# Kernel tuning notes

Hardware: AMD Instinct MI355X
Metric: run time of the kernel (lower is better)

The kernel has to match this reference:

```python
import jax, jax.numpy as jnp
import numpy as np

B = 32; SEQ = 900; GRID = 30; PFX = 16; D = 512
H = 8; HD = 64; WS = 3; SS = 1
NW = (GRID // WS) ** 2; N = WS * WS
INTER = 1536  # find_multiple(round(4.0*512*2/3), 256)
EPS = 1e-5
SCALE = HD ** -0.5


def _rel_pos_index():
    coords = np.stack(np.meshgrid(np.arange(WS), np.arange(WS), indexing='ij')).reshape(2, -1)
    rel = (coords[:, :, None] - coords[:, None, :]).transpose(1, 2, 0).copy()
    rel[:, :, 0] += WS - 1
    rel[:, :, 1] += WS - 1
    rel[:, :, 0] *= 2 * WS - 1
    return rel.sum(-1)  # [N, N]


def _attn_mask():
    img = np.zeros((GRID, GRID))
    cnt = 0
    sl = (slice(0, -WS), slice(-WS, -SS), slice(-SS, None))
    for h in sl:
        for w in sl:
            img[h, w] = cnt
            cnt += 1
    mw = img.reshape(GRID // WS, WS, GRID // WS, WS).transpose(0, 2, 1, 3).reshape(-1, N)
    diff = mw[:, None, :] - mw[:, :, None]
    return np.where(diff != 0, -100.0, 0.0).astype(np.float32)  # [nW, N, N]


REL_IDX = _rel_pos_index()
MASK = _attn_mask()


def rms_norm(x):
    xf = x.astype(jnp.float32)
    v = jnp.mean(xf * xf, -1, keepdims=True)
    return (xf * jax.lax.rsqrt(v + EPS)).astype(x.dtype)


def swiglu(x, gu_w, down_w):
    gu = x @ gu_w.T
    gate, up = gu[..., :INTER], gu[..., INTER:]
    return (jax.nn.silu(gate) * up) @ down_w.T


def setup_inputs() -> dict:
    key = jax.random.key(0)
    ks = jax.random.split(key, 8)
    s = 0.02
    return {
        'hidden_states': jax.random.normal(ks[0], (B, PFX + SEQ, D), jnp.float32),
        'qkv_w': jax.random.normal(ks[1], (3 * D, D), jnp.float32) * s,
        'qkv_b': jnp.zeros((3 * D,), jnp.float32),
        'proj_w': jax.random.normal(ks[2], (D, D), jnp.float32) * s,
        'proj_b': jnp.zeros((D,), jnp.float32),
        'rel_bias': jax.random.normal(ks[3], ((2 * WS - 1) ** 2, H), jnp.float32) * s,
        'gu_w': jax.random.normal(ks[4], (2 * INTER, D), jnp.float32) * s,
        'down_w': jax.random.normal(ks[5], (D, INTER), jnp.float32) * s,
        'pgu_w': jax.random.normal(ks[6], (2 * INTER, D), jnp.float32) * s,
        'pdown_w': jax.random.normal(ks[7], (D, INTER), jnp.float32) * s,
    }


def reference(hidden_states, qkv_w, qkv_b, proj_w, proj_b, rel_bias, gu_w, down_w, pgu_w, pdown_w):
    hs = hidden_states
    prefix = hs[:, :PFX]                                     # [B, 16, D]
    grid = hs[:, PFX:] + jnp.mean(prefix, 1, keepdims=True)  # broadcast prefix mean
    x = grid.reshape(B, GRID, GRID, D)
    residual = x
    # cyclic shift
    x = jnp.roll(x, (-SS, -SS), (1, 2))
    # window partition -> [B*nW, N, D]
    xw = x.reshape(B, GRID // WS, WS, GRID // WS, WS, D).transpose(0, 1, 3, 2, 4, 5).reshape(B * NW, N, D)
    qkv = (xw @ qkv_w.T + qkv_b).reshape(B * NW, N, 3, H, HD).transpose(2, 0, 3, 1, 4)
    q, k, v = qkv[0] * SCALE, qkv[1], qkv[2]                 # [B*nW, H, N, HD]
    attn = jnp.einsum('whid,whjd->whij', q, k)
    bias = rel_bias[jnp.asarray(REL_IDX).reshape(-1)].reshape(N, N, H).transpose(2, 0, 1)
    attn = attn + bias[None]
    attn = attn.reshape(B, NW, H, N, N) + jnp.asarray(MASK)[None, :, None]
    attn = jax.nn.softmax(attn.reshape(B * NW, H, N, N), -1)
    out = jnp.einsum('whij,whjd->whid', attn, v).transpose(0, 2, 1, 3).reshape(B * NW, N, D)
    out = out @ proj_w.T + proj_b
    # window reverse + reverse shift
    x = out.reshape(B, GRID // WS, GRID // WS, WS, WS, D).transpose(0, 1, 3, 2, 4, 5).reshape(B, GRID, GRID, D)
    x = jnp.roll(x, (SS, SS), (1, 2))
    x = rms_norm(residual.reshape(B, SEQ, D) + x.reshape(B, SEQ, D))
    prefix = rms_norm(prefix + swiglu(prefix, pgu_w, pdown_w))
    hs = jnp.concatenate([prefix, x], 1)
    return rms_norm(hs + swiglu(hs, gu_w, down_w))
```

## Files before the change

### kernel.cpp

```cpp
#include <hip/hip_runtime.h>
#include <cstdint>
#include <cstddef>

typedef float f32x4 __attribute__((ext_vector_type(4)));
typedef short s16x8 __attribute__((ext_vector_type(8)));
typedef short s16x4 __attribute__((ext_vector_type(4)));

#define DEV static __device__ __forceinline__

DEV float bf2f(short s) {
  union { unsigned u; float f; } c;
  c.u = ((unsigned)(unsigned short)s) << 16;
  return c.f;
}
DEV short f2bf(float f) {
  union { float f; unsigned u; } c;
  c.f = f;
  unsigned r = c.u + 0x7fffu + ((c.u >> 16) & 1u);
  return (short)(r >> 16);
}
DEV float wave_allsum(float v) {
#pragma unroll
  for (int off = 32; off > 0; off >>= 1) v += __shfl_xor(v, off, 64);
  return v;
}
DEV void gload_lds16(const void* g, void* l) {
  __builtin_amdgcn_global_load_lds(
      (const __attribute__((address_space(1))) void*)g,
      (__attribute__((address_space(3))) void*)l, 16, 0, 0);
}
DEV float silu_f(float g) { return g / (1.f + __expf(-g)); }

DEV int xcd_swizzle(int orig, int nwg) {
  int q = nwg >> 3, r = nwg & 7;
  int xcd = orig & 7, pos = orig >> 3;
  return (xcd < r ? xcd * (q + 1) : r * (q + 1) + (xcd - r) * q) + pos;
}

DEV void sync_phase() {
  asm volatile("s_waitcnt vmcnt(0)" ::: "memory");
  __builtin_amdgcn_s_barrier();
  __builtin_amdgcn_sched_barrier(0);
}

enum { EPI_BF16 = 0, EPI_BIAS_BF16 = 1, EPI_SCATTER = 4, EPI_GU = 6 };

template <int EPI>
__global__ __launch_bounds__(512, 2) void gemm8(
    const short* __restrict__ A, const short* __restrict__ W,
    const float* __restrict__ bias, void* __restrict__ outp,
    int M, int N, int K)
{
  __shared__ short lds[65536];
  const int tid = threadIdx.x;
  const int wid = tid >> 6, lane = tid & 63;
  const int wr = wid >> 2, wc = wid & 3;
  const int nwg = gridDim.x * gridDim.y;
  const int orig = blockIdx.y * gridDim.x + blockIdx.x;
  const int wg = xcd_swizzle(orig, nwg);
  const int bx = wg % gridDim.x, by = wg / gridDim.x;
  const int row0 = by * 256;
  const int c0 = bx * 256;

  f32x4 acc[8][4];
#pragma unroll
  for (int m = 0; m < 8; ++m)
#pragma unroll
    for (int n = 0; n < 4; ++n) acc[m][n] = f32x4{0.f, 0.f, 0.f, 0.f};

  const int srow = tid >> 3;
  const int k8s = (tid & 7) ^ (srow & 7);
  const short* aub[4];
  const short* bub[4];
#pragma unroll
  for (int u = 0; u < 4; ++u) {
    aub[u] = A + (size_t)(row0 + u * 64 + srow) * K + k8s * 8;
    bub[u] = W + (size_t)(c0 + u * 64 + srow) * K + k8s * 8;
  }
  const int ldw = wid * 512;

#define SA(d, u, kt) gload_lds16(aub[u] + (kt), &lds[(d)*16384 + (u)*4096 + ldw])
#define SB(d, u, kt) gload_lds16(bub[u] + (kt), &lds[32768 + (d)*16384 + (u)*4096 + ldw])
#define GATE(VN)                                              \
  asm volatile("s_waitcnt vmcnt(" #VN ")" ::: "memory");      \
  __builtin_amdgcn_s_barrier();                               \
  __builtin_amdgcn_sched_barrier(0);

  const int kg0 = (lane >> 4) ^ (lane & 7);
  const int kg1 = (4 + (lane >> 4)) ^ (lane & 7);
  const int aoff = (wr * 128 + (lane & 15)) * 64;
  const int boff = 32768 + (wc * 64 + (lane & 15)) * 64;

#define READ_B(d)                                                              \
  _Pragma("unroll") for (int n = 0; n < 4; ++n) {                              \
    bfr[0][n] = *(const s16x8*)&lds[(d)*16384 + boff + n * 1024 + kg0 * 8];    \
    bfr[1][n] = *(const s16x8*)&lds[(d)*16384 + boff + n * 1024 + kg1 * 8];    \
  }
#define DO_PHASE(d, p)                                                         \
  do {                                                                         \
    s16x8 a00 = *(const s16x8*)&lds[(d)*16384 + aoff + (2*(p))*1024 + kg0*8];  \
    s16x8 a01 = *(const s16x8*)&lds[(d)*16384 + aoff + (2*(p))*1024 + kg1*8];  \
    s16x8 a10 = *(const s16x8*)&lds[(d)*16384 + aoff + (2*(p)+1)*1024 + kg0*8];\
    s16x8 a11 = *(const s16x8*)&lds[(d)*16384 + aoff + (2*(p)+1)*1024 + kg1*8];\
    __builtin_amdgcn_s_setprio(1);                                             \
    _Pragma("unroll") for (int n = 0; n < 4; ++n)                              \
      acc[2*(p)][n] = __builtin_amdgcn_mfma_f32_16x16x32_bf16(a00, bfr[0][n], acc[2*(p)][n], 0, 0, 0); \
    _Pragma("unroll") for (int n = 0; n < 4; ++n)                              \
      acc[2*(p)+1][n] = __builtin_amdgcn_mfma_f32_16x16x32_bf16(a10, bfr[0][n], acc[2*(p)+1][n], 0, 0, 0); \
    _Pragma("unroll") for (int n = 0; n < 4; ++n)                              \
      acc[2*(p)][n] = __builtin_amdgcn_mfma_f32_16x16x32_bf16(a01, bfr[1][n], acc[2*(p)][n], 0, 0, 0); \
    _Pragma("unroll") for (int n = 0; n < 4; ++n)                              \
      acc[2*(p)+1][n] = __builtin_amdgcn_mfma_f32_16x16x32_bf16(a11, bfr[1][n], acc[2*(p)+1][n], 0, 0, 0); \
    __builtin_amdgcn_s_setprio(0);                                             \
  } while (0)

  SB(0, 0, 0); SB(0, 1, 0); SB(0, 2, 0); SB(0, 3, 0);
  SA(0, 0, 0); SA(0, 2, 0); SA(0, 1, 0); SA(0, 3, 0);

  const int NT = K >> 6;
  for (int t = 0; t < NT - 1; ++t) {
    const int d = t & 1, d1 = d ^ 1;
    const int kn = (t + 1) * 64;
    s16x8 bfr[2][4];
    SB(d1, 0, kn); SB(d1, 1, kn);
    GATE(4);
    READ_B(d);
    DO_PHASE(d, 0);
    SB(d1, 2, kn); SB(d1, 3, kn);
    DO_PHASE(d, 1);
    SA(d1, 0, kn); SA(d1, 2, kn);
    GATE(6);
    DO_PHASE(d, 2);
    SA(d1, 1, kn); SA(d1, 3, kn);
    DO_PHASE(d, 3);
  }
  {
    const int d = (NT - 1) & 1;
    s16x8 bfr[2][4];
    GATE(2);
    READ_B(d);
    DO_PHASE(d, 0);
    DO_PHASE(d, 1);
    GATE(0);
    DO_PHASE(d, 2);
    DO_PHASE(d, 3);
  }
#undef SA
#undef SB
#undef READ_B
#undef DO_PHASE
#undef GATE

  const int li = lane >> 4, lc = lane & 15;
#pragma unroll
  for (int m = 0; m < 8; ++m) {
#pragma unroll
    for (int i = 0; i < 4; ++i) {
      int gr = row0 + wr * 128 + m * 16 + li * 4 + i;
      if (gr >= M) continue;
      size_t orow;
      if (EPI == EPI_SCATTER) {
        int b = gr / 900, rem = gr % 900;
        int w = rem / 9, n_ = rem % 9;
        int wi = w / 10, wj = w % 10;
        int ii = n_ / 3, jj = n_ % 3;
        int gy = wi * 3 + ii + 1; if (gy >= 30) gy -= 30;
        int gx = wj * 3 + jj + 1; if (gx >= 30) gx -= 30;
        orow = (size_t)b * 900 + gy * 30 + gx;
      } else {
        orow = (size_t)gr;
      }
#pragma unroll
      for (int n = 0; n < 4; ++n) {
        int gc = c0 + wc * 64 + n * 16 + lc;
        float v = acc[m][n][i];
        if (EPI == EPI_BIAS_BF16 || EPI == EPI_SCATTER) v += bias[gc];
        ((short*)outp)[orow * (size_t)N + gc] = f2bf(v);
      }
    }
  }
}

__global__ __launch_bounds__(256, 2) void gemm8gu(
    const short* __restrict__ A, const short* __restrict__ Wg,
    const short* __restrict__ Wu, short* __restrict__ outp, int M, int K)
{
  __shared__ short lds[40960];
  const int tid = threadIdx.x;
  const int w = tid >> 6, lane = tid & 63;
  const int wr = w >> 1, wc = w & 1;
  const int nwg = gridDim.x * gridDim.y;
  const int orig = blockIdx.y * gridDim.x + blockIdx.x;
  const int wg = xcd_swizzle(orig, nwg);
  const int bx = wg % gridDim.x, by = wg / gridDim.x;
  const int row0 = by * 64;
  const int colg = bx * 128;

  f32x4 accg[2][4], accu[2][4];
#pragma unroll
  for (int m = 0; m < 2; ++m)
#pragma unroll
    for (int n = 0; n < 4; ++n) {
      accg[m][n] = f32x4{0.f, 0.f, 0.f, 0.f};
      accu[m][n] = f32x4{0.f, 0.f, 0.f, 0.f};
    }

  const short* aptr[2];
#pragma unroll
  for (int i = 0; i < 2; ++i) {
    int r = (i * 4 + w) * 8 + (lane >> 3);
    int k8 = (lane & 7) ^ (r & 7);
    aptr[i] = A + (size_t)(row0 + r) * K + k8 * 8;
  }
  const short* bptr[8];
#pragma unroll
  for (int j = 0; j < 8; ++j) {
    int br = (j * 4 + w) * 8 + (lane >> 3);
    int k8 = (lane & 7) ^ (br & 7);
    bptr[j] = (br < 128 ? Wg + (size_t)(colg + br) * K
                        : Wu + (size_t)(colg + br - 128) * K) + k8 * 8;
  }

#define SAV(d, kt)                                                         \
  do {                                                                     \
    gload_lds16(aptr[0] + (kt), &lds[(d)*4096 + w * 512]);                 \
    gload_lds16(aptr[1] + (kt), &lds[(d)*4096 + 2048 + w * 512]);          \
  } while (0)
#define SBG(d, kt)                                                         \
  do {                                                                     \
    _Pragma("unroll") for (int j = 0; j < 4; ++j)                          \
        gload_lds16(bptr[j] + (kt), &lds[8192 + (d)*16384 + (j*4 + w)*512]);\
  } while (0)
#define SBU(d, kt)                                                         \
  do {                                                                     \
    _Pragma("unroll") for (int j = 4; j < 8; ++j)                          \
        gload_lds16(bptr[j] + (kt), &lds[8192 + (d)*16384 + (j*4 + w)*512]);\
  } while (0)
#define GATE(VN)                                              \
  asm volatile("s_waitcnt vmcnt(" #VN ")" ::: "memory");      \
  __builtin_amdgcn_s_barrier();                               \
  __builtin_amdgcn_sched_barrier(0);

  const int kg0 = (lane >> 4) ^ (lane & 7);
  const int kg1 = (4 + (lane >> 4)) ^ (lane & 7);
  const int aoff = (wr * 32 + (lane & 15)) * 64;
  const int bgoff = 8192 + (wc * 64 + (lane & 15)) * 64;
  const int buoff = bgoff + 8192;

#define READ_A(d)                                                              \
  _Pragma("unroll") for (int m = 0; m < 2; ++m) {                              \
    af[0][m] = *(const s16x8*)&lds[(d)*4096 + aoff + m * 1024 + kg0 * 8];      \
    af[1][m] = *(const s16x8*)&lds[(d)*4096 + aoff + m * 1024 + kg1 * 8];      \
  }
#define READ_BF(d, BOFF, BF)                                                   \
  _Pragma("unroll") for (int n = 0; n < 4; ++n) {                              \
    BF[0][n] = *(const s16x8*)&lds[(d)*16384 + (BOFF) + n * 1024 + kg0 * 8];   \
    BF[1][n] = *(const s16x8*)&lds[(d)*16384 + (BOFF) + n * 1024 + kg1 * 8];   \
  }
#define MMH(BF, g, ACC)                                                        \
  do {                                                                         \
    __builtin_amdgcn_s_setprio(1);                                             \
    _Pragma("unroll") for (int m = 0; m < 2; ++m)                              \
        _Pragma("unroll") for (int n = 0; n < 4; ++n)                          \
            ACC[m][n] = __builtin_amdgcn_mfma_f32_16x16x32_bf16(               \
                af[g][m], BF[g][n], ACC[m][n], 0, 0, 0);                       \
    __builtin_amdgcn_s_setprio(0);                                             \
  } while (0)

  SAV(0, 0); SBG(0, 0); SBU(0, 0);

  const int NT = K >> 6;
  for (int t = 0; t < NT - 1; ++t) {
    const int d = t & 1, d1 = d ^ 1;
    const int kn = (t + 1) * 64;
    s16x8 af[2][2], bg[2][4], bu[2][4];
    GATE(4);
    READ_A(d);
    READ_BF(d, bgoff, bg);
    MMH(bg, 0, accg);
    SAV(d1, kn);
    MMH(bg, 1, accg);
    SBG(d1, kn);
    GATE(6);
    READ_BF(d, buoff, bu);
    MMH(bu, 0, accu);
    SBU(d1, kn);
    MMH(bu, 1, accu);
  }
  {
    const int d = (NT - 1) & 1;
    s16x8 af[2][2], bg[2][4], bu[2][4];
    GATE(4);
    READ_A(d);
    READ_BF(d, bgoff, bg);
    MMH(bg, 0, accg);
    MMH(bg, 1, accg);
    GATE(0);
    READ_BF(d, buoff, bu);
    MMH(bu, 0, accu);
    MMH(bu, 1, accu);
  }
#undef SAV
#undef SBG
#undef SBU
#undef READ_A
#undef READ_BF
#undef MMH
#undef GATE

  const int li = lane >> 4, lc = lane & 15;
#pragma unroll
  for (int m = 0; m < 2; ++m) {
#pragma unroll
    for (int i = 0; i < 4; ++i) {
      int gr = row0 + wr * 32 + m * 16 + li * 4 + i;
      if (gr >= M) continue;
#pragma unroll
      for (int n = 0; n < 4; ++n) {
        int gc = colg + wc * 64 + n * 16 + lc;
        outp[(size_t)gr * 1536 + gc] = f2bf(silu_f(accg[m][n][i]) * accu[m][n][i]);
      }
    }
  }
}

template <int EPI>
__global__ __launch_bounds__(256) void gemm2(
    const short* __restrict__ A, const short* __restrict__ W,
    const short* __restrict__ Wu, const float* __restrict__ bias,
    void* __restrict__ outp, int M, int N, int K)
{
  __shared__ short As0[8192], Bs0[8192];
  __shared__ short As1[8192], Bs1[8192];
  const int tid = threadIdx.x;
  const int wave = tid >> 6, lane = tid & 63;
  const int nwg = gridDim.x * gridDim.y;
  const int orig = blockIdx.y * gridDim.x + blockIdx.x;
  const int wg = xcd_swizzle(orig, nwg);
  const int bx = wg % gridDim.x, by = wg / gridDim.x;
  const int row0 = by * 128;
  const int col0 = (EPI == EPI_GU) ? bx * 64 : bx * 128;
  const int wr = wave >> 1, wc = wave & 1;

  f32x4 acc[4][4];
#pragma unroll
  for (int m = 0; m < 4; ++m)
#pragma unroll
    for (int n = 0; n < 4; ++n) acc[m][n] = f32x4{0.f, 0.f, 0.f, 0.f};

  const short* aptr[4];
  const short* bptr[4];
  int ldst[4];
#pragma unroll
  for (int i = 0; i < 4; ++i) {
    int e = i * 2048 + tid * 8;
    int srow = e >> 6;
    int skg = ((e >> 3) & 7) ^ (srow & 7);
    aptr[i] = A + (size_t)(row0 + srow) * K + skg * 8;
    if (EPI == EPI_GU)
      bptr[i] = (srow < 64 ? W + (size_t)(col0 + srow) * K
                           : Wu + (size_t)(col0 + srow - 64) * K) + skg * 8;
    else
      bptr[i] = W + (size_t)(col0 + srow) * K + skg * 8;
    ldst[i] = i * 2048 + wave * 512;
  }

#define STAGE(AS, BS, KT)                                   \
  do {                                                      \
    _Pragma("unroll") for (int i = 0; i < 4; ++i)           \
        gload_lds16(aptr[i] + (KT), &AS[ldst[i]]);          \
    _Pragma("unroll") for (int i = 0; i < 4; ++i)           \
        gload_lds16(bptr[i] + (KT), &BS[ldst[i]]);          \
  } while (0)

#define COMPUTE(AS, BS)                                                        \
  do {                                                                         \
    _Pragma("unroll") for (int ks = 0; ks < 2; ++ks) {                         \
      s16x8 af[4], bfr[4];                                                     \
      _Pragma("unroll") for (int m = 0; m < 4; ++m) {                          \
        int row = wr * 64 + m * 16 + (lane & 15);                              \
        int kg = (ks * 4 + (lane >> 4)) ^ (row & 7);                           \
        af[m] = *(const s16x8*)&AS[row * 64 + kg * 8];                         \
      }                                                                        \
      _Pragma("unroll") for (int n = 0; n < 4; ++n) {                          \
        int brow = (EPI == EPI_GU)                                             \
                       ? ((n < 2 ? wc * 32 + n * 16                            \
                                 : 64 + wc * 32 + (n - 2) * 16) + (lane & 15)) \
                       : (wc * 64 + n * 16 + (lane & 15));                     \
        int kg = (ks * 4 + (lane >> 4)) ^ (brow & 7);                          \
        bfr[n] = *(const s16x8*)&BS[brow * 64 + kg * 8];                       \
      }                                                                        \
      _Pragma("unroll") for (int m = 0; m < 4; ++m)                            \
          _Pragma("unroll") for (int n = 0; n < 4; ++n)                        \
              acc[m][n] = __builtin_amdgcn_mfma_f32_16x16x32_bf16(             \
                  af[m], bfr[n], acc[m][n], 0, 0, 0);                          \
    }                                                                          \
  } while (0)

  STAGE(As0, Bs0, 0);
  sync_phase();
  for (int kt = 0; kt < K; kt += 128) {
    STAGE(As1, Bs1, kt + 64);
    COMPUTE(As0, Bs0);
    sync_phase();
    if (kt + 128 < K) STAGE(As0, Bs0, kt + 128);
    COMPUTE(As1, Bs1);
    if (kt + 128 < K) sync_phase();
  }
#undef STAGE
#undef COMPUTE

  const int lr = (lane >> 4) * 4, lc = lane & 15;
#pragma unroll
  for (int m = 0; m < 4; ++m) {
#pragma unroll
    for (int i = 0; i < 4; ++i) {
      int gr = row0 + wr * 64 + m * 16 + lr + i;
      if (EPI == EPI_GU) {
#pragma unroll
        for (int n = 0; n < 2; ++n) {
          int gc = col0 + wc * 32 + n * 16 + lc;
          float v = silu_f(acc[m][n][i]) * acc[m][n + 2][i];
          ((short*)outp)[(size_t)gr * N + gc] = f2bf(v);
        }
      } else {
#pragma unroll
        for (int n = 0; n < 4; ++n) {
          int gc = col0 + wc * 64 + n * 16 + lc;
          ((short*)outp)[(size_t)gr * N + gc] = f2bf(acc[m][n][i]);
        }
      }
    }
  }
}

__global__ __launch_bounds__(256) void cvt_all_kernel(
    const float* __restrict__ s_qkv, const float* __restrict__ s_proj,
    const float* __restrict__ s_gu, const float* __restrict__ s_down,
    const float* __restrict__ s_pgu, const float* __restrict__ s_pdown,
    short* __restrict__ dst) {
  int i = blockIdx.x * 256 + threadIdx.x;
  if (i >= 1441792) return;
  const float* src;
  int base;
  if (i < 262144) {
    if (i < 196608) { src = s_qkv; base = 0; }
    else            { src = s_proj; base = 196608; }
  } else if (i < 851968) {
    if (i < 655360) { src = s_gu; base = 262144; }
    else            { src = s_down; base = 655360; }
  } else {
    if (i < 1245184) { src = s_pgu; base = 851968; }
    else             { src = s_pdown; base = 1245184; }
  }
  f32x4 v = *(const f32x4*)(src + (size_t)(i - base) * 4);
  s16x4 o;
#pragma unroll
  for (int e = 0; e < 4; ++e) o[e] = f2bf(v[e]);
  *(s16x4*)(dst + (size_t)i * 4) = o;
}

__global__ __launch_bounds__(256) void prefix_cvt_kernel(const float* __restrict__ hs,
                                                         short* __restrict__ dst) {
  int i = blockIdx.x * 256 + threadIdx.x;
  if (i >= 512 * 128) return;
  int r = i >> 7, c4 = i & 127;
  int b = r >> 4, t = r & 15;
  f32x4 v = *(const f32x4*)(hs + ((size_t)b * 916 + t) * 512 + c4 * 4);
  s16x4 o;
#pragma unroll
  for (int e = 0; e < 4; ++e) o[e] = f2bf(v[e]);
  *(s16x4*)(dst + (size_t)r * 512 + c4 * 4) = o;
}

__global__ __launch_bounds__(512) void mean_kernel(const float* __restrict__ hs,
                                                   float* __restrict__ m) {
  int b = blockIdx.x, d = threadIdx.x;
  float s = 0.f;
#pragma unroll
  for (int t = 0; t < 16; ++t) s += hs[((size_t)b * 916 + t) * 512 + d];
  m[b * 512 + d] = s * (1.f / 16.f);
}

__global__ __launch_bounds__(256) void prep_kernel(const float* __restrict__ hs,
                                                   const float* __restrict__ m,
                                                   short* __restrict__ xw) {
  int idx = blockIdx.x * 256 + threadIdx.x;
  if (idx >= 32 * 900 * 128) return;
  int c4 = idx & 127;
  int row = idx >> 7;
  int b = row / 900, rem = row % 900;
  int gy = rem / 30, gx = rem % 30;
  f32x4 v = *(const f32x4*)(hs + ((size_t)b * 916 + 16 + rem) * 512 + c4 * 4);
  f32x4 mm = *(const f32x4*)(m + b * 512 + c4 * 4);
  v += mm;
  int ry = gy + 29; if (ry >= 30) ry -= 30;
  int rx = gx + 29; if (rx >= 30) rx -= 30;
  int wi = ry / 3, ii = ry % 3, wj = rx / 3, jj = rx % 3;
  size_t xrow = (size_t)((b * 100 + wi * 10 + wj) * 9 + ii * 3 + jj);
  s16x4 o;
#pragma unroll
  for (int e = 0; e < 4; ++e) o[e] = f2bf(v[e]);
  *(s16x4*)(xw + xrow * 512 + c4 * 4) = o;
}

__global__ __launch_bounds__(256) void attn_kernel(const short* __restrict__ qkv,
                                                   const float* __restrict__ rel_bias,
                                                   short* __restrict__ outp) {
  __shared__ short sq[9 * 512];
  __shared__ short sk[9 * 512];
  __shared__ short sv[9 * 512];
  __shared__ float sS[648];
  const int wlin = blockIdx.x;
  const int w = wlin % 100;
  const int wi = w / 10, wj = w % 10;
  const int tid = threadIdx.x;
  const short* base = qkv + (size_t)wlin * 9 * 1536;
  for (int idx = tid; idx < 1728; idx += 256) {
    int n = idx / 192, c8 = idx % 192;
    s16x8 v = *(const s16x8*)(base + (size_t)n * 1536 + c8 * 8);
    int which = c8 >> 6;
    short* dst = (which == 0) ? sq : (which == 1) ? sk : sv;
    *(s16x8*)(dst + n * 512 + (c8 & 63) * 8) = v;
  }
  __syncthreads();
  for (int idx = tid; idx < 648; idx += 256) {
    int h = idx / 81, r = idx % 81, i = r / 9, j = r % 9;
    const short* qp = sq + i * 512 + h * 64;
    const short* kp = sk + j * 512 + h * 64;
    float dot = 0.f;
#pragma unroll
    for (int c = 0; c < 8; ++c) {
      s16x8 qv = *(const s16x8*)(qp + c * 8);
      s16x8 kv = *(const s16x8*)(kp + c * 8);
#pragma unroll
      for (int e = 0; e < 8; ++e) dot += bf2f(qv[e]) * bf2f(kv[e]);
    }
    float s = dot * 0.125f;
    int ia = i / 3, ja = i % 3, ib = j / 3, jb = j % 3;
    s += rel_bias[(5 * (ia - ib + 2) + (ja - jb + 2)) * 8 + h];
    int ra = wi * 3 + ia, ca = wj * 3 + ja, rb = wi * 3 + ib, cb = wj * 3 + jb;
    int rga = (ra < 27) ? 0 : (ra < 29) ? 1 : 2;
    int cga = (ca < 27) ? 0 : (ca < 29) ? 1 : 2;
    int rgb = (rb < 27) ? 0 : (rb < 29) ? 1 : 2;
    int cgb = (cb < 27) ? 0 : (cb < 29) ? 1 : 2;
    if (rga * 3 + cga != rgb * 3 + cgb) s -= 100.f;
    sS[idx] = s;
  }
  __syncthreads();
  if (tid < 72) {
    float* row = sS + tid * 9;
    float mx = row[0];
#pragma unroll
    for (int j = 1; j < 9; ++j) mx = fmaxf(mx, row[j]);
    float e[9], sum = 0.f;
#pragma unroll
    for (int j = 0; j < 9; ++j) { e[j] = __expf(row[j] - mx); sum += e[j]; }
    float inv = 1.f / sum;
#pragma unroll
    for (int j = 0; j < 9; ++j) row[j] = e[j] * inv;
  }
  __syncthreads();
  for (int idx = tid; idx < 576; idx += 256) {
    int h = idx / 72, r = idx % 72, i = r / 8, d8 = r % 8;
    const float* p = sS + (h * 9 + i) * 9;
    float a[8] = {0, 0, 0, 0, 0, 0, 0, 0};
#pragma unroll
    for (int j = 0; j < 9; ++j) {
      float pj = p[j];
      s16x8 vv = *(const s16x8*)(sv + j * 512 + h * 64 + d8 * 8);
#pragma unroll
      for (int e = 0; e < 8; ++e) a[e] += pj * bf2f(vv[e]);
    }
    s16x8 o;
#pragma unroll
    for (int e = 0; e < 8; ++e) o[e] = f2bf(a[e]);
    *(s16x8*)(outp + ((size_t)wlin * 9 + i) * 512 + h * 64 + d8 * 8) = o;
  }
}

__global__ __launch_bounds__(256) void addnorm1_kernel(const short* __restrict__ xw,
                                                       const short* __restrict__ p,
                                                       float* __restrict__ out,
                                                       short* __restrict__ hsb) {
  int row = blockIdx.x * 4 + (threadIdx.x >> 6);
  int lane = threadIdx.x & 63;
  int b_ = row / 900, rem = row % 900;
  int gy = rem / 30, gx = rem % 30;
  int ry = gy + 29; if (ry >= 30) ry -= 30;
  int rx = gx + 29; if (rx >= 30) rx -= 30;
  size_t xrow = (size_t)((b_ * 100 + (ry / 3) * 10 + rx / 3) * 9 + (ry % 3) * 3 + rx % 3);
  s16x8 a8 = *(const s16x8*)(xw + xrow * 512 + lane * 8);
  s16x8 b8 = *(const s16x8*)(p + (size_t)row * 512 + lane * 8);
  float x[8];
  float ss = 0.f;
#pragma unroll
  for (int e = 0; e < 8; ++e) {
    x[e] = bf2f(a8[e]) + bf2f(b8[e]);
    ss += x[e] * x[e];
  }
  ss = wave_allsum(ss);
  float sc = rsqrtf(ss * (1.f / 512.f) + 1e-5f);
  size_t orow = ((size_t)b_ * 916 + 16 + rem) * 512 + lane * 8;
  s16x8 o;
#pragma unroll
  for (int e = 0; e < 8; ++e) {
    x[e] *= sc;
    o[e] = f2bf(x[e]);
  }
  *(f32x4*)(out + orow) = f32x4{x[0], x[1], x[2], x[3]};
  *(f32x4*)(out + orow + 4) = f32x4{x[4], x[5], x[6], x[7]};
  *(s16x8*)(hsb + orow) = o;
}

__global__ __launch_bounds__(256) void prefix_addnorm_kernel(const float* __restrict__ hs,
                                                             const short* __restrict__ pd,
                                                             float* __restrict__ out,
                                                             short* __restrict__ hsb) {
  int r = blockIdx.x * 4 + (threadIdx.x >> 6);
  int lane = threadIdx.x & 63;
  int b = r >> 4, t = r & 15;
  size_t orow = ((size_t)b * 916 + t) * 512 + lane * 8;
  f32x4 a0 = *(const f32x4*)(hs + orow);
  f32x4 a1 = *(const f32x4*)(hs + orow + 4);
  s16x8 d8 = *(const s16x8*)(pd + (size_t)r * 512 + lane * 8);
  float x[8];
  float ss = 0.f;
#pragma unroll
  for (int e = 0; e < 8; ++e) {
    x[e] = (e < 4 ? a0[e] : a1[e - 4]) + bf2f(d8[e]);
    ss += x[e] * x[e];
  }
  ss = wave_allsum(ss);
  float sc = rsqrtf(ss * (1.f / 512.f) + 1e-5f);
  s16x8 o;
#pragma unroll
  for (int e = 0; e < 8; ++e) {
    x[e] *= sc;
    o[e] = f2bf(x[e]);
  }
  *(f32x4*)(out + orow) = f32x4{x[0], x[1], x[2], x[3]};
  *(f32x4*)(out + orow + 4) = f32x4{x[4], x[5], x[6], x[7]};
  *(s16x8*)(hsb + orow) = o;
}

__global__ __launch_bounds__(256) void final_addnorm_kernel(const short* __restrict__ dn,
                                                            float* __restrict__ io) {
  int row = blockIdx.x * 4 + (threadIdx.x >> 6);
  int lane = threadIdx.x & 63;
  size_t off = (size_t)row * 512 + lane * 8;
  f32x4 a0 = *(const f32x4*)(io + off);
  f32x4 a1 = *(const f32x4*)(io + off + 4);
  s16x8 d8 = *(const s16x8*)(dn + off);
  float x[8];
  float ss = 0.f;
#pragma unroll
  for (int e = 0; e < 8; ++e) {
    x[e] = (e < 4 ? a0[e] : a1[e - 4]) + bf2f(d8[e]);
    ss += x[e] * x[e];
  }
  ss = wave_allsum(ss);
  float sc = rsqrtf(ss * (1.f / 512.f) + 1e-5f);
#pragma unroll
  for (int e = 0; e < 8; ++e) x[e] *= sc;
  *(f32x4*)(io + off) = f32x4{x[0], x[1], x[2], x[3]};
  *(f32x4*)(io + off + 4) = f32x4{x[4], x[5], x[6], x[7]};
}

static constexpr size_t OFF_WQKV   = 0;
static constexpr size_t OFF_WPROJ  = 1572864;
static constexpr size_t OFF_WGU    = 2097152;
static constexpr size_t OFF_WDOWN  = 5242880;
static constexpr size_t OFF_WPGU   = 6815744;
static constexpr size_t OFF_WPDOWN = 9961472;
static constexpr size_t OFF_MEAN   = 11534336;
static constexpr size_t OFF_PREFB  = 11599872;
static constexpr size_t OFF_PINTER = 13697024;
static constexpr size_t OFF_PDOUT  = 15269888;
static constexpr size_t OFF_XW     = 16777216;
static constexpr size_t OFF_QKV    = 46399488;
static constexpr size_t OFF_ATTNO  = 134873088;
static constexpr size_t OFF_PROJS  = OFF_QKV;
static constexpr size_t OFF_INTER  = OFF_XW;
static constexpr size_t OFF_HSB    = 164364288;
static constexpr size_t OFF_DNOUT  = OFF_ATTNO;

extern "C" void kernel_launch(void* const* d_in, const int* in_sizes, int n_in,
                              void* d_out, int out_size, void* d_ws, size_t ws_size,
                              hipStream_t stream) {
  const float* hs      = (const float*)d_in[0];
  const float* qkv_w   = (const float*)d_in[1];
  const float* qkv_b   = (const float*)d_in[2];
  const float* proj_w  = (const float*)d_in[3];
  const float* proj_b  = (const float*)d_in[4];
  const float* rel_b   = (const float*)d_in[5];
  const float* gu_w    = (const float*)d_in[6];
  const float* down_w  = (const float*)d_in[7];
  const float* pgu_w   = (const float*)d_in[8];
  const float* pdown_w = (const float*)d_in[9];

  char* ws = (char*)d_ws;
  short* Wqkv   = (short*)(ws + OFF_WQKV);
  short* Wproj  = (short*)(ws + OFF_WPROJ);
  short* Wgu    = (short*)(ws + OFF_WGU);
  short* Wdown  = (short*)(ws + OFF_WDOWN);
  short* Wpgu   = (short*)(ws + OFF_WPGU);
  short* Wpdown = (short*)(ws + OFF_WPDOWN);
  float* meanb  = (float*)(ws + OFF_MEAN);
  short* prefb  = (short*)(ws + OFF_PREFB);
  short* pinter = (short*)(ws + OFF_PINTER);
  short* pdout  = (short*)(ws + OFF_PDOUT);
  short* xw     = (short*)(ws + OFF_XW);
  short* qkvb   = (short*)(ws + OFF_QKV);
  short* attno  = (short*)(ws + OFF_ATTNO);
  short* projs  = (short*)(ws + OFF_PROJS);
  short* interb = (short*)(ws + OFF_INTER);
  short* hsb    = (short*)(ws + OFF_HSB);
  short* dnout  = (short*)(ws + OFF_DNOUT);
  float* outf   = (float*)d_out;

  cvt_all_kernel<<<5632, 256, 0, stream>>>(qkv_w, proj_w, gu_w, down_w,
                                           pgu_w, pdown_w, (short*)ws);
  prefix_cvt_kernel<<<256, 256, 0, stream>>>(hs, prefb);

  mean_kernel<<<32, 512, 0, stream>>>(hs, meanb);
  prep_kernel<<<14400, 256, 0, stream>>>(hs, meanb, xw);

  gemm8<EPI_BIAS_BF16><<<dim3(6, 113), 512, 0, stream>>>(
      xw, Wqkv, qkv_b, qkvb, 28800, 1536, 512);
  attn_kernel<<<3200, 256, 0, stream>>>(qkvb, rel_b, attno);

  gemm8<EPI_SCATTER><<<dim3(2, 113), 512, 0, stream>>>(
      attno, Wproj, proj_b, projs, 28800, 512, 512);
  addnorm1_kernel<<<7200, 256, 0, stream>>>(xw, projs, outf, hsb);

  gemm2<EPI_GU><<<dim3(24, 4), 256, 0, stream>>>(
      prefb, Wpgu, Wpgu + 1536 * 512, nullptr, pinter, 512, 1536, 512);
  gemm2<EPI_BF16><<<dim3(4, 4), 256, 0, stream>>>(
      pinter, Wpdown, nullptr, nullptr, pdout, 512, 512, 1536);
  prefix_addnorm_kernel<<<128, 256, 0, stream>>>(hs, pdout, outf, hsb);

  gemm8gu<<<dim3(12, 458), 256, 0, stream>>>(
      hsb, Wgu, Wgu + 1536 * 512, interb, 29312, 512);
  gemm8<EPI_BF16><<<dim3(2, 115), 512, 0, stream>>>(
      interb, Wdown, nullptr, dnout, 29312, 512, 1536);
  final_addnorm_kernel<<<7328, 256, 0, stream>>>(dnout, outf);

  (void)in_sizes; (void)n_in; (void)out_size; (void)ws_size;
}
```

Measured before the change: 439.2 us.

## Fuse residual add and RMSNorm into full-row proj and down GEMM epilogues

Adds a gemm_norm kernel. Each block computes a 128x512 output tile covering entire rows, so the residual add and RMSNorm run in the GEMM epilogue, with a cross-wave row reduction through LDS. It replaces the proj GEMM plus addnorm1 and the down GEMM plus final_addnorm, removing two elementwise kernels and the bf16 intermediate round-trips through global memory. In exchange it runs one 512-thread block per CU with about 160KB of LDS, a simpler two-stage pipeline and roughly one wave of blocks, which may hide memory latency worse than the tuned gemm8.

```diff
diff --git a/kernel.cpp b/kernel.cpp
--- a/kernel.cpp
+++ b/kernel.cpp
@@ -43,7 +43,7 @@
   __builtin_amdgcn_sched_barrier(0);
 }
 
-enum { EPI_BF16 = 0, EPI_BIAS_BF16 = 1, EPI_SCATTER = 4, EPI_GU = 6 };
+enum { EPI_BF16 = 0, EPI_BIAS_BF16 = 1, EPI_GU = 6 };
 
 template <int EPI>
 __global__ __launch_bounds__(512, 2) void gemm8(
@@ -158,24 +158,12 @@
     for (int i = 0; i < 4; ++i) {
       int gr = row0 + wr * 128 + m * 16 + li * 4 + i;
       if (gr >= M) continue;
-      size_t orow;
-      if (EPI == EPI_SCATTER) {
-        int b = gr / 900, rem = gr % 900;
-        int w = rem / 9, n_ = rem % 9;
-        int wi = w / 10, wj = w % 10;
-        int ii = n_ / 3, jj = n_ % 3;
-        int gy = wi * 3 + ii + 1; if (gy >= 30) gy -= 30;
-        int gx = wj * 3 + jj + 1; if (gx >= 30) gx -= 30;
-        orow = (size_t)b * 900 + gy * 30 + gx;
-      } else {
-        orow = (size_t)gr;
-      }
 #pragma unroll
       for (int n = 0; n < 4; ++n) {
         int gc = c0 + wc * 64 + n * 16 + lc;
         float v = acc[m][n][i];
-        if (EPI == EPI_BIAS_BF16 || EPI == EPI_SCATTER) v += bias[gc];
-        ((short*)outp)[orow * (size_t)N + gc] = f2bf(v);
+        if (EPI == EPI_BIAS_BF16) v += bias[gc];
+        ((short*)outp)[(size_t)gr * N + gc] = f2bf(v);
       }
     }
   }
@@ -319,6 +307,145 @@
       for (int n = 0; n < 4; ++n) {
         int gc = colg + wc * 64 + n * 16 + lc;
         outp[(size_t)gr * 1536 + gc] = f2bf(silu_f(accg[m][n][i]) * accu[m][n][i]);
+      }
+    }
+  }
+}
+
+template <int PROJ>
+__global__ __launch_bounds__(512, 1) void gemm_norm(
+    const short* __restrict__ A, const short* __restrict__ W,
+    const float* __restrict__ bias, const short* __restrict__ residb,
+    float* __restrict__ outf, short* __restrict__ hsb, int K)
+{
+  __shared__ short lds[81920];
+  const int tid = threadIdx.x;
+  const int wid = tid >> 6, lane = tid & 63;
+  const int wr = wid >> 2, wc = wid & 3;
+  const int row0 = blockIdx.x * 128;
+  const int tid8 = tid * 8;
+
+  f32x4 acc[4][8];
+#pragma unroll
+  for (int m = 0; m < 4; ++m)
+#pragma unroll
+    for (int n = 0; n < 8; ++n) acc[m][n] = f32x4{0.f, 0.f, 0.f, 0.f};
+
+  const int srow = tid >> 3;
+  const int k8s = (tid & 7) ^ (srow & 7);
+  const short* aptr[2];
+#pragma unroll
+  for (int i = 0; i < 2; ++i)
+    aptr[i] = A + (size_t)(row0 + i * 64 + srow) * K + k8s * 8;
+  const short* bptr[8];
+#pragma unroll
+  for (int u = 0; u < 8; ++u)
+    bptr[u] = W + (size_t)(u * 64 + srow) * K + k8s * 8;
+
+#define STG(d, kt)                                                            \
+  do {                                                                        \
+    _Pragma("unroll") for (int i = 0; i < 2; ++i)                             \
+        gload_lds16(aptr[i] + (kt), &lds[(d)*8192 + i*4096 + tid8]);          \
+    _Pragma("unroll") for (int u = 0; u < 8; ++u)                             \
+        gload_lds16(bptr[u] + (kt), &lds[16384 + (d)*32768 + u*4096 + tid8]); \
+  } while (0)
+#define GATEN(VN)                                             \
+  asm volatile("s_waitcnt vmcnt(" #VN ")" ::: "memory");      \
+  __builtin_amdgcn_s_barrier();                               \
+  __builtin_amdgcn_sched_barrier(0);
+
+  const int kg0 = (lane >> 4) ^ (lane & 7);
+  const int kg1 = (4 + (lane >> 4)) ^ (lane & 7);
+  const int arow = (wr * 64 + (lane & 15)) * 64;
+  const int brow0 = (wc * 128 + (lane & 15)) * 64;
+
+  STG(0, 0);
+  const int NT = K >> 6;
+  for (int t = 0; t < NT; ++t) {
+    const int d = t & 1;
+    if (t + 1 < NT) {
+      STG(d ^ 1, (t + 1) * 64);
+      GATEN(10);
+    } else {
+      GATEN(0);
+    }
+    s16x8 af0[4], af1[4];
+#pragma unroll
+    for (int m = 0; m < 4; ++m) {
+      af0[m] = *(const s16x8*)&lds[d * 8192 + arow + m * 1024 + kg0 * 8];
+      af1[m] = *(const s16x8*)&lds[d * 8192 + arow + m * 1024 + kg1 * 8];
+    }
+    __builtin_amdgcn_s_setprio(1);
+#pragma unroll
+    for (int n = 0; n < 8; ++n) {
+      int bo = 16384 + d * 32768 + brow0 + n * 1024;
+      s16x8 b0 = *(const s16x8*)&lds[bo + kg0 * 8];
+      s16x8 b1 = *(const s16x8*)&lds[bo + kg1 * 8];
+#pragma unroll
+      for (int m = 0; m < 4; ++m)
+        acc[m][n] = __builtin_amdgcn_mfma_f32_16x16x32_bf16(af0[m], b0, acc[m][n], 0, 0, 0);
+#pragma unroll
+      for (int m = 0; m < 4; ++m)
+        acc[m][n] = __builtin_amdgcn_mfma_f32_16x16x32_bf16(af1[m], b1, acc[m][n], 0, 0, 0);
+    }
+    __builtin_amdgcn_s_setprio(0);
+    __builtin_amdgcn_s_barrier();
+  }
+#undef STG
+#undef GATEN
+
+  const int li = lane >> 4, lc = lane & 15;
+  float* fbuf = (float*)lds;
+#pragma unroll
+  for (int m = 0; m < 4; ++m) {
+#pragma unroll
+    for (int i = 0; i < 4; ++i) {
+      int rowl = wr * 64 + m * 16 + li * 4 + i;
+      int gr = row0 + rowl;
+      float s = 0.f;
+#pragma unroll
+      for (int n = 0; n < 8; ++n) {
+        int gc = wc * 128 + n * 16 + lc;
+        float v = acc[m][n][i];
+        if (PROJ) v += bias[gc] + bf2f(residb[(size_t)gr * 512 + gc]);
+        else      v += outf[(size_t)gr * 512 + gc];
+        acc[m][n][i] = v;
+        s += v * v;
+      }
+      s += __shfl_xor(s, 1, 64);
+      s += __shfl_xor(s, 2, 64);
+      s += __shfl_xor(s, 4, 64);
+      s += __shfl_xor(s, 8, 64);
+      if (lc == 0) fbuf[rowl * 4 + wc] = s;
+    }
+  }
+  __builtin_amdgcn_s_barrier();
+#pragma unroll
+  for (int m = 0; m < 4; ++m) {
+#pragma unroll
+    for (int i = 0; i < 4; ++i) {
+      int rowl = wr * 64 + m * 16 + li * 4 + i;
+      int gr = row0 + rowl;
+      float tot = fbuf[rowl * 4] + fbuf[rowl * 4 + 1] + fbuf[rowl * 4 + 2] + fbuf[rowl * 4 + 3];
+      float sc = rsqrtf(tot * (1.f / 512.f) + 1e-5f);
+      size_t orow;
+      if (PROJ) {
+        int b = gr / 900, rem = gr % 900;
+        int w = rem / 9, n_ = rem % 9;
+        int wi = w / 10, wj = w % 10;
+        int ii = n_ / 3, jj = n_ % 3;
+        int gy = wi * 3 + ii + 1; if (gy >= 30) gy -= 30;
+        int gx = wj * 3 + jj + 1; if (gx >= 30) gx -= 30;
+        orow = ((size_t)b * 916 + 16 + gy * 30 + gx);
+      } else {
+        orow = (size_t)gr;
+      }
+#pragma unroll
+      for (int n = 0; n < 8; ++n) {
+        int gc = wc * 128 + n * 16 + lc;
+        float v = acc[m][n][i] * sc;
+        outf[orow * 512 + gc] = v;
+        if (PROJ) hsb[orow * 512 + gc] = f2bf(v);
       }
     }
   }
@@ -579,40 +706,6 @@
   }
 }
 
-__global__ __launch_bounds__(256) void addnorm1_kernel(const short* __restrict__ xw,
-                                                       const short* __restrict__ p,
-                                                       float* __restrict__ out,
-                                                       short* __restrict__ hsb) {
-  int row = blockIdx.x * 4 + (threadIdx.x >> 6);
-  int lane = threadIdx.x & 63;
-  int b_ = row / 900, rem = row % 900;
-  int gy = rem / 30, gx = rem % 30;
-  int ry = gy + 29; if (ry >= 30) ry -= 30;
-  int rx = gx + 29; if (rx >= 30) rx -= 30;
-  size_t xrow = (size_t)((b_ * 100 + (ry / 3) * 10 + rx / 3) * 9 + (ry % 3) * 3 + rx % 3);
-  s16x8 a8 = *(const s16x8*)(xw + xrow * 512 + lane * 8);
-  s16x8 b8 = *(const s16x8*)(p + (size_t)row * 512 + lane * 8);
-  float x[8];
-  float ss = 0.f;
-#pragma unroll
-  for (int e = 0; e < 8; ++e) {
-    x[e] = bf2f(a8[e]) + bf2f(b8[e]);
-    ss += x[e] * x[e];
-  }
-  ss = wave_allsum(ss);
-  float sc = rsqrtf(ss * (1.f / 512.f) + 1e-5f);
-  size_t orow = ((size_t)b_ * 916 + 16 + rem) * 512 + lane * 8;
-  s16x8 o;
-#pragma unroll
-  for (int e = 0; e < 8; ++e) {
-    x[e] *= sc;
-    o[e] = f2bf(x[e]);
-  }
-  *(f32x4*)(out + orow) = f32x4{x[0], x[1], x[2], x[3]};
-  *(f32x4*)(out + orow + 4) = f32x4{x[4], x[5], x[6], x[7]};
-  *(s16x8*)(hsb + orow) = o;
-}
-
 __global__ __launch_bounds__(256) void prefix_addnorm_kernel(const float* __restrict__ hs,
                                                              const short* __restrict__ pd,
                                                              float* __restrict__ out,
@@ -644,29 +737,6 @@
   *(s16x8*)(hsb + orow) = o;
 }
 
-__global__ __launch_bounds__(256) void final_addnorm_kernel(const short* __restrict__ dn,
-                                                            float* __restrict__ io) {
-  int row = blockIdx.x * 4 + (threadIdx.x >> 6);
-  int lane = threadIdx.x & 63;
-  size_t off = (size_t)row * 512 + lane * 8;
-  f32x4 a0 = *(const f32x4*)(io + off);
-  f32x4 a1 = *(const f32x4*)(io + off + 4);
-  s16x8 d8 = *(const s16x8*)(dn + off);
-  float x[8];
-  float ss = 0.f;
-#pragma unroll
-  for (int e = 0; e < 8; ++e) {
-    x[e] = (e < 4 ? a0[e] : a1[e - 4]) + bf2f(d8[e]);
-    ss += x[e] * x[e];
-  }
-  ss = wave_allsum(ss);
-  float sc = rsqrtf(ss * (1.f / 512.f) + 1e-5f);
-#pragma unroll
-  for (int e = 0; e < 8; ++e) x[e] *= sc;
-  *(f32x4*)(io + off) = f32x4{x[0], x[1], x[2], x[3]};
-  *(f32x4*)(io + off + 4) = f32x4{x[4], x[5], x[6], x[7]};
-}
-
 static constexpr size_t OFF_WQKV   = 0;
 static constexpr size_t OFF_WPROJ  = 1572864;
 static constexpr size_t OFF_WGU    = 2097152;
@@ -680,10 +750,8 @@
 static constexpr size_t OFF_XW     = 16777216;
 static constexpr size_t OFF_QKV    = 46399488;
 static constexpr size_t OFF_ATTNO  = 134873088;
-static constexpr size_t OFF_PROJS  = OFF_QKV;
 static constexpr size_t OFF_INTER  = OFF_XW;
 static constexpr size_t OFF_HSB    = 164364288;
-static constexpr size_t OFF_DNOUT  = OFF_ATTNO;
 
 extern "C" void kernel_launch(void* const* d_in, const int* in_sizes, int n_in,
                               void* d_out, int out_size, void* d_ws, size_t ws_size,
@@ -713,10 +781,8 @@
   short* xw     = (short*)(ws + OFF_XW);
   short* qkvb   = (short*)(ws + OFF_QKV);
   short* attno  = (short*)(ws + OFF_ATTNO);
-  short* projs  = (short*)(ws + OFF_PROJS);
   short* interb = (short*)(ws + OFF_INTER);
   short* hsb    = (short*)(ws + OFF_HSB);
-  short* dnout  = (short*)(ws + OFF_DNOUT);
   float* outf   = (float*)d_out;
 
   cvt_all_kernel<<<5632, 256, 0, stream>>>(qkv_w, proj_w, gu_w, down_w,
@@ -730,9 +796,7 @@
       xw, Wqkv, qkv_b, qkvb, 28800, 1536, 512);
   attn_kernel<<<3200, 256, 0, stream>>>(qkvb, rel_b, attno);
 
-  gemm8<EPI_SCATTER><<<dim3(2, 113), 512, 0, stream>>>(
-      attno, Wproj, proj_b, projs, 28800, 512, 512);
-  addnorm1_kernel<<<7200, 256, 0, stream>>>(xw, projs, outf, hsb);
+  gemm_norm<1><<<225, 512, 0, stream>>>(attno, Wproj, proj_b, xw, outf, hsb, 512);
 
   gemm2<EPI_GU><<<dim3(24, 4), 256, 0, stream>>>(
       prefb, Wpgu, Wpgu + 1536 * 512, nullptr, pinter, 512, 1536, 512);
@@ -742,9 +806,8 @@
 
   gemm8gu<<<dim3(12, 458), 256, 0, stream>>>(
       hsb, Wgu, Wgu + 1536 * 512, interb, 29312, 512);
-  gemm8<EPI_BF16><<<dim3(2, 115), 512, 0, stream>>>(
-      interb, Wdown, nullptr, dnout, 29312, 512, 1536);
-  final_addnorm_kernel<<<7328, 256, 0, stream>>>(dnout, outf);
+  gemm_norm<0><<<229, 512, 0, stream>>>(interb, Wdown, nullptr, nullptr, outf,
+                                        nullptr, 1536);
 
   (void)in_sizes; (void)n_in; (void)out_size; (void)ws_size;
 }
```

After: 431.3 us. About the same (-1.8%).
